# Performance work log

Hardware: AMD Instinct MI355X
Metric: run time of the kernel (lower is better)

The kernel has to match this reference:

```python
import jax, jax.numpy as jnp
import numpy as np

B, N, C_IN, C_EMB, G = 16, 1024, 16, 64, 128
NEG = -1e12


def _lap(m):
    # m @ D^-1/2, transpose, @ D^-1/2  (matches torch code incl. transpose)
    d = jnp.sum(m, axis=1) ** -0.5
    return (m * d[None, :]).T * d[None, :]


def setup_inputs():
    key = jax.random.key(0)
    ks = jax.random.split(key, 16)
    f = jax.random.normal
    return {
        'x': f(ks[0], (B, C_IN, N), jnp.float32),
        'ct': f(ks[1], (B, C_EMB, N), jnp.float32),
        'graph_data': jax.random.uniform(ks[2], (2, N, N), dtype=jnp.float32),
        'emb_w': f(ks[3], (C_EMB, C_IN)) / np.sqrt(C_IN).astype(np.float32),
        'emb_b': f(ks[4], (C_EMB,)) * 0.01,
        'emb2_w': f(ks[5], (N, N)) / np.sqrt(N).astype(np.float32),
        'emb2_b': f(ks[6], (N,)) * 0.01,
        'att_W': f(ks[7], (C_EMB, C_EMB)) / np.sqrt(C_EMB).astype(np.float32),
        'att_a': f(ks[8], (2 * C_EMB, 1)) / np.sqrt(2 * C_EMB).astype(np.float32),
        'att_GL': f(ks[9], (N, G)) / np.sqrt(G).astype(np.float32),
        'uai_w': f(ks[10], (C_EMB, C_EMB)) / np.sqrt(C_EMB).astype(np.float32),
        'uai_b': f(ks[11], (C_EMB,)) * 0.01,
        'lin1_w': f(ks[12], (C_EMB, C_EMB)) / np.sqrt(C_EMB).astype(np.float32),
        'lin2_w': f(ks[13], (C_EMB, C_EMB)) / np.sqrt(C_EMB).astype(np.float32),
        'lin2_b': f(ks[14], (C_EMB,)) * 0.01,
        'ln_w': jnp.ones((C_EMB, N), jnp.float32),
        'ln_b': jnp.zeros((C_EMB, N), jnp.float32),
    }


def reference(x, ct, graph_data, emb_w, emb_b, emb2_w, emb2_b, att_W, att_a,
              att_GL, uai_w, uai_b, lin1_w, lin2_w, lin2_b, ln_w, ln_b):
    # emb: Conv1d k=1 -> leaky_relu -> Linear over node axis N
    h0 = jax.nn.leaky_relu(jnp.einsum('bcn,ec->ben', x, emb_w) + emb_b[None, :, None])
    h0 = jnp.einsum('ben,mn->bem', h0, emb2_w) + emb2_b[None, None, :]
    inp = jnp.swapaxes(h0, 1, 2)  # [B,N,C']

    # InterpositionAttention (repeat/cat factorized: e_ij = leakyrelu(a1.h_i + a2.h_j))
    eye = jnp.eye(N, dtype=x.dtype)
    adj_att = jax.nn.softmax(jax.nn.relu(att_GL @ att_GL.T), axis=-1) + eye
    h = inp @ att_W  # [B,N,C']
    e = jax.nn.leaky_relu((h @ att_a[:C_EMB]) + jnp.swapaxes(h @ att_a[C_EMB:], 1, 2))  # [B,N,N]
    att = jax.nn.softmax(jnp.where(adj_att > 0, e, NEG), axis=2)
    x_att = jnp.swapaxes(jax.nn.relu(att @ h), 1, 2)  # [B,C',N]

    # UAI module (eval mode: dropout off -> all MC samples equal -> sigma = 0)
    mu = jnp.swapaxes(x_att, 1, 2) @ uai_w.T + uai_b  # [B,N,C']
    x_uai = jnp.swapaxes(mu, 1, 2)  # [B,C',N]

    g1 = _lap(graph_data[0] + eye)
    g2 = _lap(graph_data[1] + eye)

    # learned adjacency from pairwise squared distances (cdist p=2, squared)
    xf = jnp.swapaxes(x_uai, 1, 2)  # [B,N,C']
    sq = jnp.sum(xf * xf, axis=-1)
    d2 = jnp.maximum(sq[:, :, None] + sq[:, None, :] - 2.0 * (xf @ jnp.swapaxes(xf, 1, 2)), 0.0)
    gl = jax.nn.softmax(jnp.exp(-d2 / (2.0 * C_EMB)) + eye, axis=-1)  # sigma^2 = emb_size

    def ln(z):  # LayerNorm over last two dims [C', N]
        m = jnp.mean(z, axis=(1, 2), keepdims=True)
        v = jnp.var(z, axis=(1, 2), keepdims=True)
        return (z - m) / jnp.sqrt(v + 1e-5) * ln_w + ln_b

    l1 = lambda z: jnp.einsum('oc,bcn->bon', lin1_w, z)
    l2 = lambda z: jnp.einsum('oc,bcn->bon', lin2_w, z) + lin2_b[None, :, None]

    x_new = ln(l1(x_uai) @ gl + l1(l1(x_uai) @ g1) @ g2)
    ft = jax.nn.gelu(ln(l2(x_uai) @ gl + l2(l2(x_uai) @ g1) @ g2), approximate=False)
    rt = ft  # rt is computed by the identical expression (dropout off)

    ct_new = ft * ct + x_new - ft * x_new
    ht = rt * jax.nn.elu(ct_new) + x_uai - rt * x_uai
    return (ht, ct_new)
```

## Files before the change

kernel.cpp:

```cpp
#include <hip/hip_runtime.h>
#include <math.h>

typedef unsigned short u16;
typedef __attribute__((ext_vector_type(8))) short short8;
typedef __attribute__((ext_vector_type(4))) float floatx4;

constexpr int BATCH = 16;
constexpr int NI = 1024;
constexpr int CE = 64;
constexpr int CI = 16;
constexpr long long NN2  = (long long)NI * NI;
constexpr long long BCN  = (long long)BATCH * CE * NI;
constexpr long long BNv  = (long long)BATCH * NI;
constexpr long long BNN  = (long long)BATCH * NI * NI;
constexpr long long S1 = (long long)CE * NI;
constexpr long long S2 = 2 * S1;
constexpr int ZERON = (int)(2 * BNv + 80);

__device__ __forceinline__ float lrelu01(float x) { return x > 0.f ? x : 0.01f * x; }

__device__ __forceinline__ u16 f2bf(float f) {
  unsigned u = __builtin_bit_cast(unsigned, f);
  return (u16)((u + 0x7fffu + ((u >> 16) & 1u)) >> 16);
}
__device__ __forceinline__ float bf2f(u16 h) {
  unsigned u = ((unsigned)h) << 16;
  return __builtin_bit_cast(float, u);
}
__device__ __forceinline__ unsigned fkey(float f) {
  unsigned u = __builtin_bit_cast(unsigned, f);
  return (u & 0x80000000u) ? ~u : (u | 0x80000000u);
}
__device__ __forceinline__ float funkey(unsigned k) {
  unsigned u = (k & 0x80000000u) ? (k & 0x7fffffffu) : ~k;
  return __builtin_bit_cast(float, u);
}

__device__ __forceinline__ void gload16(const u16* g, u16* l) {
  __builtin_amdgcn_global_load_lds(
      (const __attribute__((address_space(1))) void*)g,
      (__attribute__((address_space(3))) void*)l, 16, 0, 0);
}

__device__ __forceinline__ void pipe_fence() {
  asm volatile("s_waitcnt vmcnt(0) lgkmcnt(0)" ::: "memory");
  __builtin_amdgcn_sched_barrier(0);
  __builtin_amdgcn_s_barrier();
  __builtin_amdgcn_sched_barrier(0);
}

template<int N>
__device__ __forceinline__ void fence_bar() {
  __builtin_amdgcn_sched_barrier(0);
  if constexpr (N == 0) asm volatile("s_waitcnt vmcnt(0)" ::: "memory");
  else if constexpr (N == 1) asm volatile("s_waitcnt vmcnt(1)" ::: "memory");
  else if constexpr (N == 2) asm volatile("s_waitcnt vmcnt(2)" ::: "memory");
  else if constexpr (N == 3) asm volatile("s_waitcnt vmcnt(3)" ::: "memory");
  else if constexpr (N == 4) asm volatile("s_waitcnt vmcnt(4)" ::: "memory");
  else if constexpr (N == 6) asm volatile("s_waitcnt vmcnt(6)" ::: "memory");
  else if constexpr (N == 8) asm volatile("s_waitcnt vmcnt(8)" ::: "memory");
  else asm volatile("s_waitcnt vmcnt(0)" ::: "memory");
  __builtin_amdgcn_s_barrier();
  __builtin_amdgcn_sched_barrier(0);
}

template<int BM, int BN, int MODE>
__global__ __launch_bounds__(256) void mgemm(
    const u16* __restrict__ Ag, const u16* __restrict__ B1g, const u16* __restrict__ B2g,
    int K1, int K, int lda, int ldb, long long bsA, long long bsB1,
    float* __restrict__ Cf, u16* __restrict__ Cb, int ldc, long long bsC,
    const float* __restrict__ aux1, const float* __restrict__ aux2,
    const float* __restrict__ aux3, const float* __restrict__ aux4,
    float* __restrict__ Zout)
{
  constexpr int RM = BM / 2, RN = BN / 2, MI = RM / 16, NJ = RN / 16;
  constexpr bool PIPE3 = (MODE == 5 || MODE == 14 || MODE == 15);
  constexpr int DEPTH = (MODE == 5) ? 4 : 3;
  constexpr int NBUF = PIPE3 ? DEPTH : (MODE == 13 ? 2 : 1);
  constexpr int NLA = (BM * 8) / 256;
  constexpr int NLB = (BN * 8) / 256;
  constexpr int L = (MODE == 13) ? NLB : (NLA + NLB);
  __shared__ __align__(16) u16 As[NBUF * BM * 64];
  __shared__ __align__(16) u16 Bs[NBUF * BN * 64];
  __shared__ __align__(16) u16 xa[MODE == 13 ? 32 * 72 : 1];
  const int tid = threadIdx.x;
  int z, n0, r0, job15 = 0;
  long long cboff = 0;
  if constexpr (MODE == 15) {
    const int id = blockIdx.x;
    if (id >= 512 && id < 1536) {
      const int m = id - 512;
      float s = 0.f, sv = 0.f;
      for (int n = tid; n < NI; n += 256) {
        float g = aux3[(long long)m * NI + n] * aux2[n];
        s += g;
        sv = fmaf(g, aux1[n], sv);
      }
      float* r1 = (float*)As;
      float* r2 = (float*)As + 256;
      r1[tid] = s; r2[tid] = sv; __syncthreads();
      for (int st = 128; st > 0; st >>= 1) {
        if (tid < st) { r1[tid] += r1[tid + st]; r2[tid] += r2[tid + st]; }
        __syncthreads();
      }
      if (tid == 0) {
        float dm = aux2[m];
        Cf[m] = dm * (r1[0] + dm);
        Zout[m] = dm * (r2[0] + dm * aux1[m]);
      }
      return;
    }
    if (id >= 1536) {
      const int id2 = id - 1536;
      job15 = 2;
      z = id2 >> 5; r0 = (id2 & 1) * BM; n0 = ((id2 >> 1) & 15) * BN;
    } else {
      z = 0; n0 = (id & 15) * BN; r0 = (id >> 4) * BM;
    }
  } else if constexpr (MODE == 5) {
    const int fid = blockIdx.x;
    const int xcd = fid & 7, idx = fid >> 3;
    const int code = (idx >> 4) * 8 + xcd;
    z = code >> 1; r0 = (code & 1) * BM; n0 = (idx & 15) * BN;
  } else {
    z = blockIdx.z; n0 = blockIdx.x * BN; r0 = blockIdx.y * BM;
  }
  int Kv = K, K1v = K1, ldav = lda, ldbv = ldb;
  const u16 *Ab, *Bb1;
  if constexpr (MODE == 15) {
    if (job15 == 2) {
      Kv = 64; K1v = 128; ldav = 64; ldbv = 64;
      Ab = B2g + (long long)r0 * 64;
      Bb1 = (const u16*)aux4 + (long long)z * S1 + (long long)n0 * 64;
      cboff = bsB1 + (long long)z * S1;
    } else {
      Ab = Ag + (long long)r0 * lda;
      Bb1 = B1g + (long long)n0 * ldb;
    }
  } else {
    Ab = Ag + (long long)z * bsA + (long long)r0 * ldav;
    Bb1 = B1g + (long long)z * bsB1 + (long long)n0 * ldbv;
  }
  const int lane = tid & 63;
  const int wid = tid >> 6;
  const int wr = wid >> 1, wc = wid & 1;
  const int q = lane >> 4, mlow = lane & 15;
  const int wbase = tid & ~63;

  floatx4 acc[MI][NJ] = {};
  float zp0 = 0.f;

  float s1r_13 = 0.f, mr_13 = 0.f;
  const float* s2z_13 = nullptr;
  float4 sa, sb;
  if constexpr (MODE == 13) {
    const float* s1z = aux2 + (long long)z * NI;
    s2z_13 = aux3 + (long long)z * NI;
    const float mb = funkey(((const unsigned*)aux4)[z]);
    s1r_13 = s1z[r0 + (tid >> 3)];
    mr_13 = lrelu01(s1r_13 + mb);
  }

  auto stageAB = [&](int buf, int k0) {
    if constexpr (MODE != 13) {
      const u16* Asrc = Ab + k0;
#pragma unroll
      for (int s = 0; s < NLA; s++) {
        int cid = tid + s * 256;
        int r = cid >> 3, cc = cid & 7;
        gload16(Asrc + (long long)r * ldav + ((cc ^ (r & 7)) << 3),
                As + buf * (BM * 64) + ((wbase + s * 256) << 3));
      }
    }
    const u16* Bsrc = (k0 < K1v) ? (Bb1 + k0)
                                 : (B2g + (long long)n0 * ldbv + (k0 - K1v));
#pragma unroll
    for (int s = 0; s < NLB; s++) {
      int cid = tid + s * 256;
      int r = cid >> 3, cc = cid & 7;
      gload16(Bsrc + (long long)r * ldbv + ((cc ^ (r & 7)) << 3),
              Bs + buf * (BN * 64) + ((wbase + s * 256) << 3));
    }
  };

  auto agen_ld = [&](int k0) {
    const float* sp = s2z_13 + k0 + (tid & 7) * 8;
    sa = *(const float4*)sp;
    sb = *(const float4*)(sp + 4);
  };
  auto agen_st = [&](int buf) {
    int r = tid >> 3, craw = tid & 7;
    float p0 = __expf(lrelu01(s1r_13 + sa.x) - mr_13);
    float p1 = __expf(lrelu01(s1r_13 + sa.y) - mr_13);
    float p2 = __expf(lrelu01(s1r_13 + sa.z) - mr_13);
    float p3 = __expf(lrelu01(s1r_13 + sa.w) - mr_13);
    float p4 = __expf(lrelu01(s1r_13 + sb.x) - mr_13);
    float p5 = __expf(lrelu01(s1r_13 + sb.y) - mr_13);
    float p6 = __expf(lrelu01(s1r_13 + sb.z) - mr_13);
    float p7 = __expf(lrelu01(s1r_13 + sb.w) - mr_13);
    zp0 += p0 + p1 + p2 + p3 + p4 + p5 + p6 + p7;
    uint4 v;
    v.x = (unsigned)f2bf(p0) | ((unsigned)f2bf(p1) << 16);
    v.y = (unsigned)f2bf(p2) | ((unsigned)f2bf(p3) << 16);
    v.z = (unsigned)f2bf(p4) | ((unsigned)f2bf(p5) << 16);
    v.w = (unsigned)f2bf(p6) | ((unsigned)f2bf(p7) << 16);
    *(uint4*)&As[buf * (BM * 64) + (r * 8 + (craw ^ (r & 7))) * 8] = v;
  };

  auto compute_tile = [&](int buf) {
#pragma unroll
    for (int kh = 0; kh < 2; kh++) {
      const int kc = kh * 4 + q;
      short8 afr[MI], bfr[NJ];
#pragma unroll
      for (int i = 0; i < MI; i++) {
        int row = wr * RM + i * 16 + mlow;
        afr[i] = *(const short8*)&As[buf * (BM * 64) + (row * 8 + (kc ^ (row & 7))) * 8];
      }
#pragma unroll
      for (int j = 0; j < NJ; j++) {
        int row = wc * RN + j * 16 + mlow;
        bfr[j] = *(const short8*)&Bs[buf * (BN * 64) + (row * 8 + (kc ^ (row & 7))) * 8];
      }
#pragma unroll
      for (int i = 0; i < MI; i++)
#pragma unroll
        for (int j = 0; j < NJ; j++)
          acc[i][j] = __builtin_amdgcn_mfma_f32_16x16x32_bf16(afr[i], bfr[j], acc[i][j], 0, 0, 0);
    }
  };

  if constexpr (PIPE3) {
    const int nk = Kv >> 6;
#pragma unroll
    for (int p = 0; p < DEPTH - 1; p++) stageAB(p, p << 6);
    fence_bar<(DEPTH - 2) * L>();
    int cur = 0, stg = DEPTH - 1;
    for (int ki = 0; ki < nk; ki++) {
      if (ki + DEPTH - 1 < nk) stageAB(stg, (ki + DEPTH - 1) << 6);
      compute_tile(cur);
      if (ki + 1 < nk) {
        const int rem = nk - 1 - ki;
        const int u = (rem < DEPTH - 1) ? rem : (DEPTH - 1);
        if constexpr (DEPTH == 4) {
          if (u == 3) fence_bar<2 * L>();
          else if (u == 2) fence_bar<L>();
          else fence_bar<0>();
        } else {
          if (u == 2) fence_bar<L>();
          else fence_bar<0>();
        }
      }
      cur++; if (cur == NBUF) cur = 0;
      stg++; if (stg == NBUF) stg = 0;
    }
    __syncthreads();
  } else if constexpr (MODE == 13) {
    agen_ld(0);
    stageAB(0, 0);
    agen_st(0);
    pipe_fence();
    int cur = 0;
    for (int k0 = 0; k0 < Kv; k0 += 64) {
      if (k0 + 64 < Kv) {
        agen_ld(k0 + 64);
        stageAB(cur ^ 1, k0 + 64);
        agen_st(cur ^ 1);
      }
      compute_tile(cur);
      pipe_fence();
      cur ^= 1;
    }
  } else {
    for (int k0 = 0; k0 < Kv; k0 += 64) {
      stageAB(0, k0);
      __syncthreads();
      compute_tile(0);
      __syncthreads();
    }
  }

  if constexpr (MODE == 3) {
    const float* sqb = aux1 + (long long)z * NI;
#pragma unroll
    for (int i = 0; i < MI; i++) {
#pragma unroll
      for (int rg = 0; rg < 4; rg++) {
        int r = r0 + wr * RM + i * 16 + q * 4 + rg;
        float sqi = sqb[r];
        float rsum = 0.f;
#pragma unroll
        for (int j = 0; j < NJ; j++) {
          int ncol = n0 + wc * RN + j * 16 + mlow;
          float d2 = fmaxf(sqi + sqb[ncol] - 2.f * acc[i][j][rg], 0.f);
          float w = __expf(__expf(-d2 * (1.f / 128.f)) + (r == ncol ? 1.f : 0.f) - 2.f);
          Cb[(long long)z * bsC + (long long)r * ldc + ncol] = f2bf(w);
          rsum += w;
        }
        rsum += __shfl_xor(rsum, 1);
        rsum += __shfl_xor(rsum, 2);
        rsum += __shfl_xor(rsum, 4);
        rsum += __shfl_xor(rsum, 8);
        if (mlow == 0) atomicAdd(&Zout[(long long)z * NI + r], rsum);
      }
    }
  } else if constexpr (MODE == 14) {
    float ps1 = 0.f, ps2 = 0.f;
#pragma unroll
    for (int i = 0; i < MI; i++) {
#pragma unroll
      for (int rg = 0; rg < 4; rg++) {
        int r = wr * RM + i * 16 + q * 4 + rg;
        int ncol = n0 + wc * RN + mlow;
        float v = acc[i][0][rg] + aux3[r] * aux1[ncol];
        Cb[(long long)z * bsC + (long long)r * ldc + ncol] = f2bf(v);
        ps1 = fmaf(v, aux2[r], ps1);
        ps2 = fmaf(v, aux2[64 + r], ps2);
      }
    }
    ps1 += __shfl_xor(ps1, 16); ps1 += __shfl_xor(ps1, 32);
    ps2 += __shfl_xor(ps2, 16); ps2 += __shfl_xor(ps2, 32);
    float* sred = (float*)As;
    const int col = wc * RN + mlow;
    if (q == 0) { sred[col * 2 + wr] = ps1; sred[64 + col * 2 + wr] = ps2; }
    __syncthreads();
    if (tid < 32) {
      float v1 = sred[tid * 2] + sred[tid * 2 + 1];
      float v2 = sred[64 + tid * 2] + sred[64 + tid * 2 + 1];
      Cf[(long long)z * NI + n0 + tid] = v1;
      Zout[(long long)z * NI + n0 + tid] = v2;
      float mx = v2;
      for (int off = 1; off < 32; off <<= 1) mx = fmaxf(mx, __shfl_xor(mx, off));
      if (tid == 0) atomicMax((unsigned*)B2g + z, fkey(mx));
    }
  } else if constexpr (MODE == 13) {
    float* zred = (float*)xa;
    float* zinv = (float*)xa + 256;
    zred[(tid >> 3) * 8 + (tid & 7)] = zp0;
    __syncthreads();
    if (tid < 32) {
      float sum = 0.f;
#pragma unroll
      for (int j = 0; j < 8; j++) sum += zred[tid * 8 + j];
      zinv[tid] = 1.f / sum;
    }
    __syncthreads();
    float zr[4];
#pragma unroll
    for (int rg = 0; rg < 4; rg++) zr[rg] = zinv[wr * 16 + q * 4 + rg];
    __syncthreads();
#pragma unroll
    for (int j = 0; j < NJ; j++) {
#pragma unroll
      for (int rg = 0; rg < 4; rg++) {
        int row = wr * 16 + q * 4 + rg;
        int col = wc * RN + j * 16 + mlow;
        float v = fmaxf(acc[0][j][rg] * zr[rg], 0.f);
        xa[row * 72 + col] = f2bf(v);
      }
    }
#pragma unroll
    for (int s = 0; s < 2; s++) {
      int cid = tid + s * 256;
      int r = cid >> 3, cc = cid & 7;
      gload16(B2g + r * 64 + ((cc ^ (r & 7)) << 3),
              Bs + ((wbase + s * 256) << 3));
    }
    __syncthreads();
    floatx4 acc2[2] = {};
#pragma unroll
    for (int kh = 0; kh < 2; kh++) {
      const int kc = kh * 4 + q;
      short8 a2 = *(const short8*)&xa[(wr * 16 + mlow) * 72 + kc * 8];
#pragma unroll
      for (int j = 0; j < 2; j++) {
        int orow = wc * 32 + j * 16 + mlow;
        short8 b2 = *(const short8*)&Bs[(orow * 8 + (kc ^ (orow & 7))) * 8];
        acc2[j] = __builtin_amdgcn_mfma_f32_16x16x32_bf16(a2, b2, acc2[j], 0, 0, 0);
      }
    }
#pragma unroll
    for (int rg = 0; rg < 4; rg++) {
      int row = r0 + wr * 16 + q * 4 + rg;
      float sqp = 0.f;
#pragma unroll
      for (int j = 0; j < 2; j++) {
        int o = wc * 32 + j * 16 + mlow;
        float v = acc2[j][rg] + aux1[o];
        Cb[(long long)z * bsC + (long long)row * ldc + o] = f2bf(v);
        sqp = fmaf(v, v, sqp);
      }
      sqp += __shfl_xor(sqp, 1);
      sqp += __shfl_xor(sqp, 2);
      sqp += __shfl_xor(sqp, 4);
      sqp += __shfl_xor(sqp, 8);
      if (mlow == 0) atomicAdd(&Zout[(long long)z * NI + row], sqp);
    }
  } else if constexpr (MODE == 5) {
    float ts = 0.f, tss = 0.f;
#pragma unroll
    for (int i = 0; i < MI; i++) {
#pragma unroll
      for (int j = 0; j < NJ; j++) {
#pragma unroll
        for (int rg = 0; rg < 4; rg++) {
          int r = r0 + wr * RM + i * 16 + q * 4 + rg;
          int ncol = n0 + wc * RN + j * 16 + mlow;
          float v = acc[i][j][rg];
          v += aux3[r] * aux1[ncol] + aux4[r] * aux2[ncol];
          Cb[(long long)z * bsC + (long long)r * ldc + ncol] = f2bf(v);
          ts += v;
          tss = fmaf(v, v, tss);
        }
      }
    }
    float* red = (float*)As;
    red[tid] = ts; red[256 + tid] = tss;
    __syncthreads();
    for (int st = 128; st > 0; st >>= 1) {
      if (tid < st) { red[tid] += red[tid + st]; red[256 + tid] += red[256 + tid + st]; }
      __syncthreads();
    }
    if (tid == 0) {
      const int half = r0 >> 6;
      atomicAdd(&Zout[z * 2 + half], red[0]);
      atomicAdd(&Zout[32 + z * 2 + half], red[256]);
    }
  } else {
#pragma unroll
    for (int i = 0; i < MI; i++) {
#pragma unroll
      for (int j = 0; j < NJ; j++) {
#pragma unroll
        for (int rg = 0; rg < 4; rg++) {
          int r = r0 + wr * RM + i * 16 + q * 4 + rg;
          int ncol = n0 + wc * RN + j * 16 + mlow;
          float v = acc[i][j][rg];
          if constexpr (MODE == 4) {
            int blk = r >> 6, oo = r & 63;
            int drow = ((blk & 1) << 6) + oo;
            if (blk < 2) v = (v + aux3[drow]) / aux1[(long long)z * NI + ncol];
            Cb[(long long)z * bsC + (long long)drow * 2048 + (long long)(blk >> 1) * 1024 + ncol] =
                f2bf(v);
          } else if constexpr (MODE == 15) {
            Cb[cboff + (long long)r * ldc + ncol] = f2bf(v);
          } else {
            Cb[(long long)z * bsC + (long long)r * ldc + ncol] = f2bf(v);
          }
        }
      }
    }
  }
}

__global__ __launch_bounds__(256) void lap_rowsum(const float* __restrict__ gd,
                                                  float* __restrict__ dr,
                                                  float* __restrict__ zero)
{
  if (blockIdx.x >= 2048) {
    int i = (blockIdx.x - 2048) * 256 + threadIdx.x;
    if (i < ZERON) zero[i] = 0.f;
    return;
  }
  const int ki = blockIdx.x;
  const float* row = gd + (long long)ki * NI;
  float s = 0.f;
  for (int j = threadIdx.x; j < NI; j += 256) s += row[j];
  __shared__ float red[256];
  red[threadIdx.x] = s; __syncthreads();
  for (int st = 128; st > 0; st >>= 1) {
    if (threadIdx.x < st) red[threadIdx.x] += red[threadIdx.x + st];
    __syncthreads();
  }
  if (threadIdx.x == 0) dr[ki] = rsqrtf(red[0] + 1.f);
}

__global__ __launch_bounds__(256) void mega_prep(
    const float* __restrict__ l1w, const float* __restrict__ l2w,
    const float* __restrict__ l2b, const float* __restrict__ uaiw,
    const float* __restrict__ attW,
    u16* __restrict__ stack4, float* __restrict__ rb2ext, float* __restrict__ rl2ext,
    u16* __restrict__ uaiw_bf, u16* __restrict__ attwT_bf, float* __restrict__ wcs,
    const float* __restrict__ emb2w, u16* __restrict__ emb2w_bf,
    const float* __restrict__ x, const float* __restrict__ ew,
    const float* __restrict__ eb, u16* __restrict__ h0aT,
    const float* __restrict__ gd, const float* __restrict__ dsum,
    u16* __restrict__ g2t, u16* __restrict__ g1,
    float* __restrict__ cs1)
{
  __shared__ float sm[1092];
  const int bid = blockIdx.x;
  const int t = threadIdx.x;
  if (bid < 98) {
    const int gid = bid * 256 + t;
    if (gid < 4096) {
      stack4[gid] = f2bf(l1w[gid]);
    } else if (gid < 8192) {
      stack4[gid] = f2bf(l2w[gid - 4096]);
    } else if (gid < 12288) {
      int tt = gid - 8192, o = tt >> 6, m = tt & 63;
      float s = 0.f;
      for (int c = 0; c < 64; c++) s = fmaf(l1w[o * 64 + c], l1w[c * 64 + m], s);
      stack4[gid] = f2bf(s);
    } else if (gid < 16384) {
      int tt = gid - 12288, o = tt >> 6, m = tt & 63;
      float s = 0.f;
      for (int c = 0; c < 64; c++) s = fmaf(l2w[o * 64 + c], l2w[c * 64 + m], s);
      stack4[gid] = f2bf(s);
    } else if (gid < 16512) {
      int r = gid - 16384;
      rb2ext[r] = (r < 64) ? 0.f : l2b[r - 64];
    } else if (gid < 16640) {
      int r = gid - 16512;
      float v = 0.f;
      if (r >= 64) { int o = r - 64; for (int c = 0; c < 64; c++) v = fmaf(l2w[o * 64 + c], l2b[c], v); }
      rl2ext[r] = v;
    } else if (gid < 20736) {
      uaiw_bf[gid - 16640] = f2bf(uaiw[gid - 16640]);
    } else if (gid < 24832) {
      int idx = gid - 20736;
      int c = idx >> 6, e = idx & 63;
      attwT_bf[idx] = f2bf(attW[e * 64 + c]);
    } else if (gid < 24896) {
      int c = gid - 24832;
      float s = 0.f;
      for (int e = 0; e < 64; e++) s += attW[e * 64 + c];
      wcs[c] = s;
    }
  } else if (bid < 4194) {
    const long long i = (long long)(bid - 98) * 256 + t;
    emb2w_bf[i] = f2bf(emb2w[i]);
  } else if (bid < 4450) {
    const int sub = bid - 4194;
    const int b = sub >> 4;
    const int nc = (sub & 15) * 64;
    float* we = sm;
    float* be = sm + 1024;
    for (int i = t; i < 1024; i += 256) we[i] = ew[i];
    if (t < 64) be[t] = eb[t];
    __syncthreads();
    const int n = nc + (t >> 2);
    const int e0 = (t & 3) * 16;
    const float* xb = x + (long long)b * CI * NI + n;
    float xv[16];
#pragma unroll
    for (int c = 0; c < CI; c++) xv[c] = xb[(long long)c * NI];
    u16 out16[16];
#pragma unroll
    for (int ee = 0; ee < 16; ee++) {
      const int e = e0 + ee;
      float a = be[e];
#pragma unroll
      for (int c = 0; c < CI; c++) a = fmaf(xv[c], we[e * 16 + c], a);
      out16[ee] = f2bf(lrelu01(a));
    }
    u16* dst = h0aT + (long long)b * S1 + (long long)n * 64 + e0;
    *(uint4*)dst = *(uint4*)out16;
    *(uint4*)(dst + 8) = *(uint4*)(out16 + 8);
  } else if (bid < 8546) {
    const long long idx = (long long)(bid - 4450) * 256 + t;
    const int m = (int)(idx >> 10), j = (int)(idx & 1023);
    const float* d = dsum + NI;
    float v = (gd[NN2 + idx] + (m == j ? 1.f : 0.f)) * d[m] * d[j];
    g2t[idx] = f2bf(v);
  } else if (bid < 9570) {
    const int sub = bid - 8546;
    const int bx = (sub & 31) * 32, by = (sub >> 5) * 32;
    const int lx = t & 31, ly = t >> 5;
    float* tile = sm;
    for (int yy = ly; yy < 32; yy += 8)
      tile[yy * 33 + lx] = gd[(long long)(by + yy) * NI + bx + lx];
    __syncthreads();
    for (int yy = ly; yy < 32; yy += 8) {
      const int i = bx + yy, j = by + lx;
      float v = (tile[lx * 33 + yy] + (i == j ? 1.f : 0.f)) * dsum[i] * dsum[j];
      g1[(long long)i * NI + j] = f2bf(v);
    }
  } else {
    const int n = bid - 9570;
    float s = 0.f;
    for (int i = t; i < NI; i += 256) s = fmaf(gd[(long long)n * NI + i], dsum[i], s);
    float* red = sm;
    red[t] = s; __syncthreads();
    for (int st = 128; st > 0; st >>= 1) {
      if (t < st) red[t] += red[t + st];
      __syncthreads();
    }
    if (t == 0) cs1[n] = dsum[n] * (red[0] + dsum[n]);
  }
}

__global__ __launch_bounds__(512) void ln_final_t(const u16* __restrict__ T,
                                                  const float* __restrict__ stats,
                                                  const float* __restrict__ lnw,
                                                  const float* __restrict__ lnb,
                                                  const float* __restrict__ ct,
                                                  const u16* __restrict__ xuT,
                                                  float* __restrict__ outp)
{
  __shared__ float xs[64 * 65];
  const int blk = blockIdx.x;
  const int b = blk >> 4;
  const int n0 = (blk & 15) << 6;
  const int t = threadIdx.x;
  const int tc = t & 63, tr = t >> 6;
#pragma unroll
  for (int i = 0; i < 8; i++) {
    int nn = i * 8 + tr;
    xs[tc * 65 + nn] = bf2f(xuT[((long long)b << 16) + (long long)(n0 + nn) * 64 + tc]);
  }
  __syncthreads();
  const float inv_n = 1.f / 65536.f;
  const float m0 = stats[b * 2] * inv_n;
  const float m1 = stats[b * 2 + 1] * inv_n;
  const float rs0 = rsqrtf(fmaxf(stats[32 + b * 2] * inv_n - m0 * m0, 0.f) + 1e-5f);
  const float rs1 = rsqrtf(fmaxf(stats[32 + b * 2 + 1] * inv_n - m1 * m1, 0.f) + 1e-5f);
#pragma unroll
  for (int j = 0; j < 8; j++) {
    const int c = j * 8 + tr;
    const int n = n0 + tc;
    const int rem = c * NI + n;
    const long long toff = (long long)b * S2 + rem;
    const float t0 = bf2f(T[toff]);
    const float t1 = bf2f(T[toff + S1]);
    const float w = lnw[rem], bb = lnb[rem];
    const float xn = (t0 - m0) * rs0 * w + bb;
    float ft = (t1 - m1) * rs1 * w + bb;
    ft = 0.5f * ft * (1.f + erff(ft * 0.70710678118654752f));
    const float u = xs[c * 65 + tc];
    const long long oidx = ((long long)b << 16) + rem;
    const float cn = fmaf(ft, ct[oidx] - xn, xn);
    const float el = cn > 0.f ? cn : expm1f(cn);
    outp[oidx] = fmaf(ft, el - u, u);
    outp[BCN + oidx] = cn;
  }
}

extern "C" void kernel_launch(void* const* d_in, const int* in_sizes, int n_in,
                              void* d_out, int out_size, void* d_ws, size_t ws_size,
                              hipStream_t stream)
{
  (void)in_sizes; (void)n_in; (void)out_size; (void)ws_size;
  const float* x      = (const float*)d_in[0];
  const float* ct     = (const float*)d_in[1];
  const float* gdata  = (const float*)d_in[2];
  const float* emb_w  = (const float*)d_in[3];
  const float* emb_b  = (const float*)d_in[4];
  const float* emb2_w = (const float*)d_in[5];
  const float* emb2_b = (const float*)d_in[6];
  const float* att_W  = (const float*)d_in[7];
  const float* att_a  = (const float*)d_in[8];
  const float* uai_w  = (const float*)d_in[10];
  const float* uai_b  = (const float*)d_in[11];
  const float* lin1_w = (const float*)d_in[12];
  const float* lin2_w = (const float*)d_in[13];
  const float* lin2_b = (const float*)d_in[14];
  const float* ln_w   = (const float*)d_in[15];
  const float* ln_b   = (const float*)d_in[16];
  float* outp = (float*)d_out;

  float* ws = (float*)d_ws;
  long long o = 0;
  auto af = [&](long long n) { float* p = ws + o; o += (n + 63) & ~63LL; return p; };
  auto au = [&](long long n) { return (u16*)af((n + 1) / 2); };

  float* s1      = af(BNv);
  float* s2      = af(BNv);
  float* dsum    = af(2 * NI);
  float* cs1v    = af(NI);
  float* cs2v    = af(NI);
  float* v2v     = af(NI);
  float* rb2ext  = af(128);
  float* rl2ext  = af(128);
  float* wcs     = af(64);
  float* zeroreg = af(ZERON);
  float* Zgl     = zeroreg;
  float* sqv     = zeroreg + BNv;
  float* stats   = zeroreg + 2 * BNv;
  unsigned* s2mU = (unsigned*)(stats + 64);
  u16* Tacc      = au(S2 * BATCH);
  u16* emb2w_bf  = au(NN2);
  u16* h0aTb     = au(S1 * BATCH);
  u16* ybf       = au(S1 * BATCH);
  u16* hTb       = au(S1 * BATCH);
  u16* xuaiTb    = au(S1 * BATCH);
  u16* g1b       = au(NN2);
  u16* g2tb      = au(NN2);
  u16* G12b      = au(NN2);
  u16* Abig      = au((long long)BATCH * 128 * 2048);
  u16* stack4    = au(256 * 64);
  u16* uaiw_bf   = au(CE * CE);
  u16* attwT_bf  = au(CE * CE);
  u16* bigW      = au(BNN);

  lap_rowsum<<<2048 + (ZERON + 255) / 256, 256, 0, stream>>>(gdata, dsum, zeroreg);

  mega_prep<<<10594, 256, 0, stream>>>(
      lin1_w, lin2_w, lin2_b, uai_w, att_W,
      stack4, rb2ext, rl2ext, uaiw_bf, attwT_bf, wcs,
      emb2_w, emb2w_bf, x, emb_w, emb_b, h0aTb,
      gdata, dsum, g2tb, g1b, cs1v);

  mgemm<32, 64, 15><<<2048, 256, 0, stream>>>(
      g2tb, g1b, attwT_bf, NI, NI, NI, NI, 0, (long long)(ybf - G12b),
      cs2v, G12b, NI, 0, cs1v, dsum + NI, gdata + NN2, (const float*)h0aTb, v2v);

  mgemm<64, 32, 14><<<dim3(32, 1, BATCH), 256, 0, stream>>>(
      ybf, emb2w_bf, (const u16*)s2mU, NI, NI, NI, NI, S1, 0,
      s1, hTb, NI, S1, emb2_b, att_a, wcs, nullptr, s2);

  mgemm<32, 64, 13><<<dim3(1, 32, BATCH), 256, 0, stream>>>(
      hTb, hTb, uaiw_bf, NI, NI, NI, NI, 0, S1,
      nullptr, xuaiTb, CE, S1, uai_b, s1, s2, (const float*)s2mU, sqv);

  mgemm<64, 64, 3><<<dim3(16, 16, 16), 256, 0, stream>>>(
      xuaiTb, xuaiTb, nullptr, CE, CE, CE, CE, S1, S1,
      nullptr, bigW, NI, NN2, sqv, nullptr, nullptr, nullptr, Zgl);

  mgemm<64, 64, 4><<<dim3(16, 4, BATCH), 256, 0, stream>>>(
      stack4, xuaiTb, nullptr, CE, CE, CE, CE, 0, S1,
      nullptr, Abig, 0, (long long)128 * 2048, Zgl, nullptr, rb2ext, nullptr, nullptr);

  mgemm<64, 64, 5><<<512, 256, 0, stream>>>(
      Abig, bigW, G12b, NI, 2 * NI, 2048, NI, (long long)128 * 2048, NN2,
      nullptr, Tacc, NI, S2, cs2v, v2v, rb2ext, rl2ext, stats);

  ln_final_t<<<256, 512, 0, stream>>>(Tacc, stats, ln_w, ln_b, ct, xuaiTb, outp);
}
```

Before: 224.6 us.

## Retile GEMM stages, add XCD-aware block mapping, deepen mode-13 pipeline, fuse mode-4 half

Several changes land together. Modes 13, 14 and 3 switch to a 1D grid with XCD-aware block-to-batch mapping. Mode 13 gets a triple-buffered B pipeline with a partial vmcnt wait instead of a full drain. The Z-independent half of the mode-4 GEMM moves into the mode-3 launch as extra blocks, so mode 4 now covers only two row-blocks. Mode 5 drops from 64x64 with 4-deep buffering to 64x32 tiles with 3-deep buffering over twice as many blocks. The goal is better L2 locality, more occupancy and overlap, and one less serialized launch, at the cost of more complex indexing and more blocks.

```diff
diff --git a/kernel.cpp b/kernel.cpp
--- a/kernel.cpp
+++ b/kernel.cpp
@@ -42,9 +42,9 @@
       (__attribute__((address_space(3))) void*)l, 16, 0, 0);
 }
 
-__device__ __forceinline__ void pipe_fence() {
-  asm volatile("s_waitcnt vmcnt(0) lgkmcnt(0)" ::: "memory");
+__device__ __forceinline__ void fence13() {
   __builtin_amdgcn_sched_barrier(0);
+  asm volatile("s_waitcnt vmcnt(2) lgkmcnt(0)" ::: "memory");
   __builtin_amdgcn_s_barrier();
   __builtin_amdgcn_sched_barrier(0);
 }
@@ -75,16 +75,18 @@
 {
   constexpr int RM = BM / 2, RN = BN / 2, MI = RM / 16, NJ = RN / 16;
   constexpr bool PIPE3 = (MODE == 5 || MODE == 14 || MODE == 15);
-  constexpr int DEPTH = (MODE == 5) ? 4 : 3;
-  constexpr int NBUF = PIPE3 ? DEPTH : (MODE == 13 ? 2 : 1);
+  constexpr int DEPTH = 3;
+  constexpr int NBB = PIPE3 ? DEPTH : (MODE == 13 ? 3 : 1);
+  constexpr int NBA = PIPE3 ? DEPTH : (MODE == 13 ? 2 : 1);
   constexpr int NLA = (BM * 8) / 256;
   constexpr int NLB = (BN * 8) / 256;
   constexpr int L = (MODE == 13) ? NLB : (NLA + NLB);
-  __shared__ __align__(16) u16 As[NBUF * BM * 64];
-  __shared__ __align__(16) u16 Bs[NBUF * BN * 64];
+  __shared__ __align__(16) u16 As[NBA * BM * 64];
+  __shared__ __align__(16) u16 Bs[NBB * BN * 64];
   __shared__ __align__(16) u16 xa[MODE == 13 ? 32 * 72 : 1];
   const int tid = threadIdx.x;
   int z, n0, r0, job15 = 0;
+  bool job4 = false;
   long long cboff = 0;
   if constexpr (MODE == 15) {
     const int id = blockIdx.x;
@@ -120,8 +122,29 @@
   } else if constexpr (MODE == 5) {
     const int fid = blockIdx.x;
     const int xcd = fid & 7, idx = fid >> 3;
-    const int code = (idx >> 4) * 8 + xcd;
-    z = code >> 1; r0 = (code & 1) * BM; n0 = (idx & 15) * BN;
+    const int code = (idx >> 5) * 8 + xcd;
+    z = code >> 1; r0 = (code & 1) * BM; n0 = (idx & 31) * BN;
+  } else if constexpr (MODE == 3) {
+    const int id = blockIdx.x;
+    if (id < 4096) {
+      const int xcd = id & 7, idx = id >> 3;
+      z = (idx >> 8) * 8 + xcd;
+      const int g = idx & 255;
+      n0 = (g & 15) * 64; r0 = ((g >> 4) & 15) * 64;
+    } else {
+      const int t = id - 4096;
+      job4 = true;
+      z = t >> 5;
+      const int yblk = 2 + ((t >> 4) & 1);
+      r0 = yblk * 64;
+      n0 = (t & 15) * 64;
+    }
+  } else if constexpr (MODE == 13 || MODE == 14) {
+    const int id = blockIdx.x;
+    const int xcd = id & 7, idx = id >> 3;
+    z = (idx >> 5) * 8 + xcd;
+    if constexpr (MODE == 13) { r0 = (idx & 31) * BM; n0 = 0; }
+    else { n0 = (idx & 31) * BN; r0 = 0; }
   } else {
     z = blockIdx.z; n0 = blockIdx.x * BN; r0 = blockIdx.y * BM;
   }
@@ -140,6 +163,9 @@
   } else {
     Ab = Ag + (long long)z * bsA + (long long)r0 * ldav;
     Bb1 = B1g + (long long)z * bsB1 + (long long)n0 * ldbv;
+    if constexpr (MODE == 3) {
+      if (job4) Ab = ((const u16*)aux2) + (long long)r0 * 64;
+    }
   }
   const int lane = tid & 63;
   const int wid = tid >> 6;
@@ -207,7 +233,7 @@
     *(uint4*)&As[buf * (BM * 64) + (r * 8 + (craw ^ (r & 7))) * 8] = v;
   };
 
-  auto compute_tile = [&](int buf) {
+  auto compute_tile = [&](int bufA, int bufB) {
 #pragma unroll
     for (int kh = 0; kh < 2; kh++) {
       const int kc = kh * 4 + q;
@@ -215,12 +241,12 @@
 #pragma unroll
       for (int i = 0; i < MI; i++) {
         int row = wr * RM + i * 16 + mlow;
-        afr[i] = *(const short8*)&As[buf * (BM * 64) + (row * 8 + (kc ^ (row & 7))) * 8];
+        afr[i] = *(const short8*)&As[bufA * (BM * 64) + (row * 8 + (kc ^ (row & 7))) * 8];
       }
 #pragma unroll
       for (int j = 0; j < NJ; j++) {
         int row = wc * RN + j * 16 + mlow;
-        bfr[j] = *(const short8*)&Bs[buf * (BN * 64) + (row * 8 + (kc ^ (row & 7))) * 8];
+        bfr[j] = *(const short8*)&Bs[bufB * (BN * 64) + (row * 8 + (kc ^ (row & 7))) * 8];
       }
 #pragma unroll
       for (int i = 0; i < MI; i++)
@@ -233,75 +259,89 @@
   if constexpr (PIPE3) {
     const int nk = Kv >> 6;
 #pragma unroll
-    for (int p = 0; p < DEPTH - 1; p++) stageAB(p, p << 6);
+    for (int p = 0; p < DEPTH - 1; p++) {
+      int kk = (p < nk) ? p : (nk - 1);
+      stageAB(p, kk << 6);
+    }
     fence_bar<(DEPTH - 2) * L>();
     int cur = 0, stg = DEPTH - 1;
     for (int ki = 0; ki < nk; ki++) {
       if (ki + DEPTH - 1 < nk) stageAB(stg, (ki + DEPTH - 1) << 6);
-      compute_tile(cur);
+      compute_tile(cur, cur);
       if (ki + 1 < nk) {
         const int rem = nk - 1 - ki;
         const int u = (rem < DEPTH - 1) ? rem : (DEPTH - 1);
-        if constexpr (DEPTH == 4) {
-          if (u == 3) fence_bar<2 * L>();
-          else if (u == 2) fence_bar<L>();
-          else fence_bar<0>();
-        } else {
-          if (u == 2) fence_bar<L>();
-          else fence_bar<0>();
-        }
-      }
-      cur++; if (cur == NBUF) cur = 0;
-      stg++; if (stg == NBUF) stg = 0;
+        if (u == 2) fence_bar<L>();
+        else fence_bar<0>();
+      }
+      cur++; if (cur == NBB) cur = 0;
+      stg++; if (stg == NBB) stg = 0;
     }
     __syncthreads();
   } else if constexpr (MODE == 13) {
+    const int nk = Kv >> 6;
     agen_ld(0);
     stageAB(0, 0);
+    if (nk > 1) stageAB(1, 64);
     agen_st(0);
-    pipe_fence();
-    int cur = 0;
-    for (int k0 = 0; k0 < Kv; k0 += 64) {
-      if (k0 + 64 < Kv) {
-        agen_ld(k0 + 64);
-        stageAB(cur ^ 1, k0 + 64);
-        agen_st(cur ^ 1);
-      }
-      compute_tile(cur);
-      pipe_fence();
-      cur ^= 1;
+    fence13();
+    for (int ki = 0; ki < nk; ki++) {
+      if (ki + 1 < nk) agen_ld((ki + 1) << 6);
+      if (ki + 2 < nk) stageAB((ki + 2) % 3, (ki + 2) << 6);
+      if (ki + 1 < nk) agen_st((ki + 1) & 1);
+      compute_tile(ki & 1, ki % 3);
+      fence13();
     }
   } else {
     for (int k0 = 0; k0 < Kv; k0 += 64) {
       stageAB(0, k0);
       __syncthreads();
-      compute_tile(0);
+      compute_tile(0, 0);
       __syncthreads();
     }
   }
 
   if constexpr (MODE == 3) {
-    const float* sqb = aux1 + (long long)z * NI;
-#pragma unroll
-    for (int i = 0; i < MI; i++) {
-#pragma unroll
-      for (int rg = 0; rg < 4; rg++) {
-        int r = r0 + wr * RM + i * 16 + q * 4 + rg;
-        float sqi = sqb[r];
-        float rsum = 0.f;
+    if (job4) {
+      u16* abig = (u16*)Cf;
+#pragma unroll
+      for (int i = 0; i < MI; i++) {
 #pragma unroll
         for (int j = 0; j < NJ; j++) {
-          int ncol = n0 + wc * RN + j * 16 + mlow;
-          float d2 = fmaxf(sqi + sqb[ncol] - 2.f * acc[i][j][rg], 0.f);
-          float w = __expf(__expf(-d2 * (1.f / 128.f)) + (r == ncol ? 1.f : 0.f) - 2.f);
-          Cb[(long long)z * bsC + (long long)r * ldc + ncol] = f2bf(w);
-          rsum += w;
+#pragma unroll
+          for (int rg = 0; rg < 4; rg++) {
+            int r = r0 + wr * RM + i * 16 + q * 4 + rg;
+            int ncol = n0 + wc * RN + j * 16 + mlow;
+            int blk = r >> 6, oo = r & 63;
+            int drow = ((blk & 1) << 6) + oo;
+            abig[(long long)z * (128 * 2048LL) + (long long)drow * 2048 + 1024 + ncol] =
+                f2bf(acc[i][j][rg]);
+          }
         }
-        rsum += __shfl_xor(rsum, 1);
-        rsum += __shfl_xor(rsum, 2);
-        rsum += __shfl_xor(rsum, 4);
-        rsum += __shfl_xor(rsum, 8);
-        if (mlow == 0) atomicAdd(&Zout[(long long)z * NI + r], rsum);
+      }
+    } else {
+      const float* sqb = aux1 + (long long)z * NI;
+#pragma unroll
+      for (int i = 0; i < MI; i++) {
+#pragma unroll
+        for (int rg = 0; rg < 4; rg++) {
+          int r = r0 + wr * RM + i * 16 + q * 4 + rg;
+          float sqi = sqb[r];
+          float rsum = 0.f;
+#pragma unroll
+          for (int j = 0; j < NJ; j++) {
+            int ncol = n0 + wc * RN + j * 16 + mlow;
+            float d2 = fmaxf(sqi + sqb[ncol] - 2.f * acc[i][j][rg], 0.f);
+            float w = __expf(__expf(-d2 * (1.f / 128.f)) + (r == ncol ? 1.f : 0.f) - 2.f);
+            Cb[(long long)z * bsC + (long long)r * ldc + ncol] = f2bf(w);
+            rsum += w;
+          }
+          rsum += __shfl_xor(rsum, 1);
+          rsum += __shfl_xor(rsum, 2);
+          rsum += __shfl_xor(rsum, 4);
+          rsum += __shfl_xor(rsum, 8);
+          if (mlow == 0) atomicAdd(&Zout[(long long)z * NI + r], rsum);
+        }
       }
     }
   } else if constexpr (MODE == 14) {
@@ -705,23 +745,23 @@
       g2tb, g1b, attwT_bf, NI, NI, NI, NI, 0, (long long)(ybf - G12b),
       cs2v, G12b, NI, 0, cs1v, dsum + NI, gdata + NN2, (const float*)h0aTb, v2v);
 
-  mgemm<64, 32, 14><<<dim3(32, 1, BATCH), 256, 0, stream>>>(
+  mgemm<64, 32, 14><<<512, 256, 0, stream>>>(
       ybf, emb2w_bf, (const u16*)s2mU, NI, NI, NI, NI, S1, 0,
       s1, hTb, NI, S1, emb2_b, att_a, wcs, nullptr, s2);
 
-  mgemm<32, 64, 13><<<dim3(1, 32, BATCH), 256, 0, stream>>>(
+  mgemm<32, 64, 13><<<512, 256, 0, stream>>>(
       hTb, hTb, uaiw_bf, NI, NI, NI, NI, 0, S1,
       nullptr, xuaiTb, CE, S1, uai_b, s1, s2, (const float*)s2mU, sqv);
 
-  mgemm<64, 64, 3><<<dim3(16, 16, 16), 256, 0, stream>>>(
+  mgemm<64, 64, 3><<<4608, 256, 0, stream>>>(
       xuaiTb, xuaiTb, nullptr, CE, CE, CE, CE, S1, S1,
-      nullptr, bigW, NI, NN2, sqv, nullptr, nullptr, nullptr, Zgl);
-
-  mgemm<64, 64, 4><<<dim3(16, 4, BATCH), 256, 0, stream>>>(
+      (float*)Abig, bigW, NI, NN2, sqv, (const float*)stack4, nullptr, nullptr, Zgl);
+
+  mgemm<64, 64, 4><<<dim3(16, 2, BATCH), 256, 0, stream>>>(
       stack4, xuaiTb, nullptr, CE, CE, CE, CE, 0, S1,
       nullptr, Abig, 0, (long long)128 * 2048, Zgl, nullptr, rb2ext, nullptr, nullptr);
 
-  mgemm<64, 64, 5><<<512, 256, 0, stream>>>(
+  mgemm<64, 32, 5><<<1024, 256, 0, stream>>>(
       Abig, bigW, G12b, NI, 2 * NI, 2048, NI, (long long)128 * 2048, NN2,
       nullptr, Tacc, NI, S2, cs2v, v2v, rb2ext, rl2ext, stats);
 
```

After: 225.8 us. Within noise of the previous version (+0.6%).
